# Performance work log

Measured on AMD Instinct MI355X. Metric: run time of the kernel, lower is better.

## Reference

```python
import jax, jax.numpy as jnp
import numpy as np

S, D = 16384, 1024


def setup_inputs() -> dict:
    key = jax.random.key(0)
    ks = jax.random.split(key, 7)
    stdv = 1.0 / np.sqrt(D)
    u = lambda k, shape: jax.random.uniform(k, shape, jnp.float32, -stdv, stdv)
    return {
        "x": jax.random.normal(ks[0], (S, D), jnp.float32),
        "Wq": u(ks[1], (D, D)), "bq": u(ks[2], (D,)),
        "Wk": u(ks[3], (D, D)), "bk": u(ks[4], (D,)),
        "Wv": u(ks[5], (D, D)), "bv": u(ks[6], (D,)),
    }


def reference(x, Wq, bq, Wk, bk, Wv, bv):
    # torch.nn.Linear: y = x @ W^T + b
    q = x @ Wq.T + bq          # [S, D]
    k = x @ Wk.T + bk          # [S, D]
    v = x @ Wv.T + bv          # [S, D]
    d = x.shape[-1]
    # NOTE: faithful to source -- scores are over the FEATURE axis: [D, D]
    scores = jnp.einsum('sd,se->de', q, k) / jnp.sqrt(jnp.float32(d))
    attn = jax.nn.softmax(scores, axis=-1)   # [D, D]
    out = v @ attn                           # [S, D]
    return out, attn
```

## Files before the change

### kernel.cpp

```cpp
#include <hip/hip_runtime.h>
#include <hip/hip_bf16.h>
#include <stdint.h>


#define S_ 16384
#define D_ 1024

typedef _Float16 half8 __attribute__((ext_vector_type(8)));
typedef _Float16 half4 __attribute__((ext_vector_type(4)));
typedef float f32x4 __attribute__((ext_vector_type(4)));

__device__ __forceinline__ void gload_lds16(const _Float16* g, _Float16* l) {
    __builtin_amdgcn_global_load_lds(
        (const __attribute__((address_space(1))) void*)g,
        (__attribute__((address_space(3))) void*)l, 16, 0, 0);
}

#define VM4() asm volatile("s_waitcnt vmcnt(4)" ::: "memory")
#define BARR() do { __builtin_amdgcn_s_barrier(); __builtin_amdgcn_sched_barrier(0); } while (0)
#define LGKM0() do { asm volatile("s_waitcnt lgkmcnt(0)" ::: "memory"); __builtin_amdgcn_sched_barrier(0); } while (0)

#define STAGEA(H, KT, NX) do { \
    const _Float16* _s = srcA + (size_t)((H) * 128) * lda + (size_t)(KT) * 64; \
    _Float16* _d = AsS + (NX) * 16384 + ((H) * 128 + 8 * w) * 64; \
    gload_lds16(_s, _d); \
    gload_lds16(_s + (size_t)64 * lda, _d + 4096); \
} while (0)

#define STAGEB(H, KT, NX) do { \
    const _Float16* _s = srcB + (size_t)((H) * 128) * ldb + (size_t)(KT) * 64; \
    _Float16* _d = BsS + (NX) * 16384 + ((H) * 128 + 8 * w) * 64; \
    gload_lds16(_s, _d); \
    gload_lds16(_s + (size_t)64 * ldb, _d + 4096); \
} while (0)

#define READA(QA) do { _Pragma("unroll") \
    for (int fm = 0; fm < 4; ++fm) { \
        af[fm][0] = *(const half8*)(pA + (((QA) * 64 + fm * 16) << 7) + cx0); \
        af[fm][1] = *(const half8*)(pA + (((QA) * 64 + fm * 16) << 7) + cx1); } \
} while (0)

#define READB(BF, QB) do { _Pragma("unroll") \
    for (int fn = 0; fn < 2; ++fn) { \
        BF[fn][0] = *(const half8*)(pB + (((QB) * 32 + fn * 16) << 7) + cx0); \
        BF[fn][1] = *(const half8*)(pB + (((QB) * 32 + fn * 16) << 7) + cx1); } \
} while (0)

#define MFMAB(QA, QB, BF) do { _Pragma("unroll") \
    for (int fm = 0; fm < 4; ++fm) { _Pragma("unroll") \
        for (int fn = 0; fn < 2; ++fn) { \
            f32x4 _c = acc[(QA) * 4 + fm][(QB) * 2 + fn]; \
            _c = __builtin_amdgcn_mfma_f32_16x16x32_f16(af[fm][0], BF[fn][0], _c, 0, 0, 0); \
            _c = __builtin_amdgcn_mfma_f32_16x16x32_f16(af[fm][1], BF[fn][1], _c, 0, 0, 0); \
            acc[(QA) * 4 + fm][(QB) * 2 + fn] = _c; } } \
} while (0)

template <int F16OUT, int BIAS>
__global__ __launch_bounds__(512, 2)
void gemm256(const _Float16* __restrict__ A, const _Float16* __restrict__ B,
             void* __restrict__ C, const float* __restrict__ bias,
             int lda, int ldb, int ldc, int ksub, long long mn,
             int ntx, int ntxy, int cpx) {
    __shared__ _Float16 As[2][16384];
    __shared__ _Float16 Bs[2][16384];
    const int t = threadIdx.x;
    const int l = t & 63;
    const int w = t >> 6;
    const int wm = w >> 2, wn = w & 3;

    const int hb = blockIdx.x;
    const int lg = (hb & 7) * cpx + (hb >> 3);
    const int bz = lg / ntxy;
    const int rem = lg - bz * ntxy;
    const int by = rem / ntx;
    const int bx = rem - by * ntx;
    const size_t m0 = (size_t)by * 256;
    const size_t n0 = (size_t)bx * 256;
    const size_t k0 = (size_t)bz * (size_t)ksub;
    const long long coff = (long long)bz * mn;

    const int colsw = 8 * ((l & 7) ^ (l >> 3));
    const _Float16* srcA = A + (m0 + 8 * w + (l >> 3)) * (size_t)lda + k0 + colsw;
    const _Float16* srcB = B + (n0 + 8 * w + (l >> 3)) * (size_t)ldb + k0 + colsw;
    _Float16* AsS = &As[0][0];
    _Float16* BsS = &Bs[0][0];

    const int cx0 = (((l >> 4) << 4)) ^ ((l & 7) << 4);
    const int cx1 = (64 + ((l >> 4) << 4)) ^ ((l & 7) << 4);
    const char* basePA = (const char*)AsS + (wm * 128 + (l & 15)) * 128;
    const char* basePB = (const char*)BsS + (wn * 64 + (l & 15)) * 128;

    f32x4 acc[8][4] = {};
    half8 af[4][2], bf0[2][2], bf1[2][2];

    const int nk = ksub >> 6;

    STAGEA(0, 0, 0); STAGEB(0, 0, 0); STAGEB(1, 0, 0); STAGEA(1, 0, 0);

    for (int kt = 0; kt < nk; ++kt) {
        const int p = kt & 1, nx = p ^ 1;
        const int ktn = kt + 1;
        const bool hn = ktn < nk;
        const char* pA = basePA + p * 32768;
        const char* pB = basePB + p * 32768;

        VM4(); BARR();
        READA(0); READB(bf0, 0);
        if (hn) STAGEA(0, ktn, nx);
        LGKM0();
        __builtin_amdgcn_s_setprio(1);
        MFMAB(0, 0, bf0);
        __builtin_amdgcn_s_setprio(0);

        VM4(); BARR();
        READB(bf1, 1);
        if (hn) STAGEB(0, ktn, nx);
        LGKM0();
        __builtin_amdgcn_s_setprio(1);
        MFMAB(0, 1, bf1);
        __builtin_amdgcn_s_setprio(0);

        VM4(); BARR();
        READA(1);
        if (hn) { STAGEB(1, ktn, nx); STAGEA(1, ktn, nx); }
        LGKM0();
        __builtin_amdgcn_s_setprio(1);
        MFMAB(1, 0, bf0);
        MFMAB(1, 1, bf1);
        __builtin_amdgcn_s_setprio(0);
    }

    const int cr = (l >> 4) << 2;
    const int cc = l & 15;
#pragma unroll
    for (int n = 0; n < 4; ++n) {
        const size_t col = n0 + wn * 64 + n * 16 + cc;
        const float bb = BIAS ? bias[col] : 0.f;
#pragma unroll
        for (int m = 0; m < 8; ++m) {
            const size_t row0 = m0 + wm * 128 + m * 16 + cr;
#pragma unroll
            for (int r = 0; r < 4; ++r) {
                const float val = acc[m][n][r] + bb;
                if (F16OUT)
                    ((_Float16*)C)[coff + (long long)(row0 + r) * ldc + col] = (_Float16)val;
                else
                    ((float*)C)[coff + (long long)(row0 + r) * ldc + col] = val;
            }
        }
    }
}

__global__ __launch_bounds__(256, 2)
void gemm_abt(const _Float16* __restrict__ A, const _Float16* __restrict__ B,
              float* __restrict__ C, const float* __restrict__ bias,
              int bias_mode, int lda, int ldb, int ldc, int ksub,
              float scale, long long mn) {
    const int t = threadIdx.x;
    const int lane = t & 63;
    const int wave = t >> 6;
    const int wr = (wave >> 1) * 64;
    const int wc = (wave & 1) * 64;
    const size_t m0 = (size_t)blockIdx.y * 128;
    const size_t n0 = (size_t)blockIdx.x * 128;
    const size_t k0 = (size_t)blockIdx.z * (size_t)ksub;
    const long long coff = (long long)blockIdx.z * mn;

    __shared__ _Float16 As[128 * 32];
    __shared__ _Float16 Bs[128 * 32];

    f32x4 acc[4][4] = {};

    const _Float16* a0 = A + (m0 + (size_t)(t >> 2)) * (size_t)lda + k0 + (t & 3) * 8;
    const _Float16* a1 = a0 + (size_t)64 * lda;
    const _Float16* b0 = B + (n0 + (size_t)(t >> 2)) * (size_t)ldb + k0 + (t & 3) * 8;
    const _Float16* b1 = b0 + (size_t)64 * ldb;
    _Float16* AsW0 = As + wave * 512;
    _Float16* AsW1 = As + 2048 + wave * 512;
    _Float16* BsW0 = Bs + wave * 512;
    _Float16* BsW1 = Bs + 2048 + wave * 512;

    const int nk = ksub >> 5;
    for (int kt = 0; kt < nk; ++kt) {
        __syncthreads();
        gload_lds16(a0, AsW0);
        gload_lds16(a1, AsW1);
        gload_lds16(b0, BsW0);
        gload_lds16(b1, BsW1);
        a0 += 32; a1 += 32; b0 += 32; b1 += 32;
        __syncthreads();

        half8 af[4], bf[4];
#pragma unroll
        for (int i = 0; i < 4; ++i)
            af[i] = *(const half8*)(As + (wr + i * 16 + (lane & 15)) * 32 + (lane >> 4) * 8);
#pragma unroll
        for (int i = 0; i < 4; ++i)
            bf[i] = *(const half8*)(Bs + (wc + i * 16 + (lane & 15)) * 32 + (lane >> 4) * 8);
#pragma unroll
        for (int i = 0; i < 4; ++i)
#pragma unroll
            for (int j = 0; j < 4; ++j)
                acc[i][j] = __builtin_amdgcn_mfma_f32_16x16x32_f16(af[i], bf[j], acc[i][j], 0, 0, 0);
    }

    const int cr = (lane >> 4) * 4;
    const int cc = lane & 15;
#pragma unroll
    for (int i = 0; i < 4; ++i) {
#pragma unroll
        for (int j = 0; j < 4; ++j) {
            const size_t row0 = m0 + wr + i * 16 + cr;
            const size_t col = n0 + wc + j * 16 + cc;
            const float bcol = (bias_mode == 2) ? bias[col] : 0.f;
#pragma unroll
            for (int r = 0; r < 4; ++r) {
                float val = acc[i][j][r] * scale + bcol;
                C[coff + (long long)(row0 + r) * ldc + col] = val;
            }
        }
    }
}

__global__ void cast_f32_f16(const float* __restrict__ in, _Float16* __restrict__ out, int n8) {
    int i = blockIdx.x * 256 + threadIdx.x;
    if (i >= n8) return;
    const f32x4* p = (const f32x4*)in + (size_t)i * 2;
    f32x4 x0 = p[0], x1 = p[1];
    half8 h;
    h[0] = (_Float16)x0[0]; h[1] = (_Float16)x0[1];
    h[2] = (_Float16)x0[2]; h[3] = (_Float16)x0[3];
    h[4] = (_Float16)x1[0]; h[5] = (_Float16)x1[1];
    h[6] = (_Float16)x1[2]; h[7] = (_Float16)x1[3];
    ((half8*)out)[i] = h;
}

template <int WRITE_ROW, int COLSUM>
__global__ __launch_bounds__(256)
void cast_transpose(const float* __restrict__ in, _Float16* __restrict__ outRow,
                    _Float16* __restrict__ outT, float* __restrict__ msum, int ldT) {
    __shared__ _Float16 tile[64][66];
    __shared__ float red[16][16][4];
    const int t = threadIdx.x;
    const int c0 = blockIdx.x * 64;
    const int r0 = blockIdx.y * 64;
    const int cg = t & 15;
    const int rb = t >> 4;
    f32x4 csum = {};
#pragma unroll
    for (int it = 0; it < 4; ++it) {
        const int rr = rb + it * 16;
        f32x4 v = *(const f32x4*)(in + (size_t)(r0 + rr) * 1024 + c0 + cg * 4);
        if (COLSUM) { csum[0] += v[0]; csum[1] += v[1]; csum[2] += v[2]; csum[3] += v[3]; }
        _Float16 h0 = (_Float16)v[0], h1 = (_Float16)v[1];
        _Float16 h2 = (_Float16)v[2], h3 = (_Float16)v[3];
        tile[rr][cg * 4 + 0] = h0; tile[rr][cg * 4 + 1] = h1;
        tile[rr][cg * 4 + 2] = h2; tile[rr][cg * 4 + 3] = h3;
        if (WRITE_ROW) {
            half4 h = {h0, h1, h2, h3};
            *(half4*)(outRow + (size_t)(r0 + rr) * 1024 + c0 + cg * 4) = h;
        }
    }
    if (COLSUM) {
        red[rb][cg][0] = csum[0]; red[rb][cg][1] = csum[1];
        red[rb][cg][2] = csum[2]; red[rb][cg][3] = csum[3];
    }
    __syncthreads();
    if (COLSUM && t < 64) {
        float s = 0.f;
#pragma unroll
        for (int k = 0; k < 16; ++k) s += red[k][t >> 2][t & 3];
        atomicAdd(msum + c0 + t, s);
    }
    const int i = t >> 2, ch = (t & 3) * 16;
    half8 h0v, h1v;
#pragma unroll
    for (int j = 0; j < 8; ++j) h0v[j] = tile[ch + j][i];
#pragma unroll
    for (int j = 0; j < 8; ++j) h1v[j] = tile[ch + 8 + j][i];
    *(half8*)(outT + (size_t)(c0 + i) * ldT + r0 + ch) = h0v;
    *(half8*)(outT + (size_t)(c0 + i) * ldT + r0 + ch + 8) = h1v;
}

__global__ void zero_vec(float* __restrict__ p, int n) {
    int i = blockIdx.x * 256 + threadIdx.x;
    if (i < n) p[i] = 0.f;
}

__global__ __launch_bounds__(256)
void u2w_kernel(const float* __restrict__ Wq, const float* __restrict__ Wk,
                const float* __restrict__ bq, const float* __restrict__ m,
                float* __restrict__ u2, float* __restrict__ w) {
    const int bid = blockIdx.x;
    const int t = threadIdx.x;
    const float* W = (bid < 1024) ? Wq : Wk;
    const int row = (bid < 1024) ? bid : bid - 1024;
    float s = 0.f;
#pragma unroll
    for (int it = 0; it < 4; ++it) {
        const int i = t + it * 256;
        s += W[(size_t)row * 1024 + i] * m[i];
    }
    for (int o = 32; o; o >>= 1) s += __shfl_xor(s, o);
    __shared__ float red[4];
    if ((t & 63) == 0) red[t >> 6] = s;
    __syncthreads();
    if (t == 0) {
        float tot = red[0] + red[1] + red[2] + red[3];
        if (bid < 1024) u2[bid] = tot + 16384.0f * bq[bid];
        else w[row] = tot;
    }
}

__global__ __launch_bounds__(256)
void reduce_g(const _Float16* __restrict__ part, _Float16* __restrict__ G16) {
    const size_t off = ((size_t)blockIdx.x * 256 + threadIdx.x) * 8;
    float s[8] = {};
    for (int z = 0; z < 16; ++z) {
        half8 v = *(const half8*)(part + (size_t)z * 1048576 + off);
#pragma unroll
        for (int j = 0; j < 8; ++j) s[j] += (float)v[j];
    }
    half8 o;
#pragma unroll
    for (int j = 0; j < 8; ++j) o[j] = (_Float16)s[j];
    *(half8*)(G16 + off) = o;
}

__global__ __launch_bounds__(256)
void reduce_cast(const float* __restrict__ part, _Float16* __restrict__ outh,
                 int nz, float scale) {
    const int idx = (blockIdx.x * 256 + threadIdx.x) * 4;
    f32x4 s = {};
    for (int z = 0; z < nz; ++z) {
        f32x4 v = *(const f32x4*)(part + (size_t)z * 1048576 + idx);
        s[0] += v[0]; s[1] += v[1]; s[2] += v[2]; s[3] += v[3];
    }
    half4 h;
    h[0] = (_Float16)(s[0] * scale); h[1] = (_Float16)(s[1] * scale);
    h[2] = (_Float16)(s[2] * scale); h[3] = (_Float16)(s[3] * scale);
    *(half4*)(outh + idx) = h;
}

__global__ __launch_bounds__(256)
void softmax_rows(const float* __restrict__ part, const float* __restrict__ u2,
                  const float* __restrict__ bq, const float* __restrict__ bk,
                  const float* __restrict__ w,
                  float* __restrict__ P, _Float16* __restrict__ PT) {
    const int a = blockIdx.x;
    const int t = threadIdx.x;
    __shared__ float red[8];
    const size_t off = (size_t)a * 1024 + t * 4;
    f32x4 s = {};
#pragma unroll
    for (int z = 0; z < 4; ++z) {
        f32x4 v = *(const f32x4*)(part + (size_t)z * 1048576 + off);
        s[0] += v[0]; s[1] += v[1]; s[2] += v[2]; s[3] += v[3];
    }
    const float ru = u2[a], rb = bq[a];
    f32x4 bk4 = *(const f32x4*)(bk + t * 4);
    f32x4 w4 = *(const f32x4*)(w + t * 4);
#pragma unroll
    for (int j = 0; j < 4; ++j) s[j] = (s[j] + ru * bk4[j] + rb * w4[j]) * 0.03125f;

    float m = fmaxf(fmaxf(s[0], s[1]), fmaxf(s[2], s[3]));
    for (int o = 32; o; o >>= 1) m = fmaxf(m, __shfl_xor(m, o));
    if ((t & 63) == 0) red[t >> 6] = m;
    __syncthreads();
    m = fmaxf(fmaxf(red[0], red[1]), fmaxf(red[2], red[3]));

    float e0 = expf(s[0] - m), e1 = expf(s[1] - m);
    float e2 = expf(s[2] - m), e3 = expf(s[3] - m);
    float sum = e0 + e1 + e2 + e3;
    for (int o = 32; o; o >>= 1) sum += __shfl_xor(sum, o);
    if ((t & 63) == 0) red[4 + (t >> 6)] = sum;
    __syncthreads();
    sum = red[4] + red[5] + red[6] + red[7];
    const float inv = 1.0f / sum;

    f32x4 o4 = {e0 * inv, e1 * inv, e2 * inv, e3 * inv};
    *(f32x4*)(P + off) = o4;
    const int b = t * 4;
    PT[(size_t)(b + 0) * 1024 + a] = (_Float16)o4[0];
    PT[(size_t)(b + 1) * 1024 + a] = (_Float16)o4[1];
    PT[(size_t)(b + 2) * 1024 + a] = (_Float16)o4[2];
    PT[(size_t)(b + 3) * 1024 + a] = (_Float16)o4[3];
}

__global__ __launch_bounds__(256)
void attn_bv(const float* __restrict__ attn, const float* __restrict__ bv,
             float* __restrict__ c) {
    const int j = blockIdx.x * 256 + threadIdx.x;
    const int a0 = blockIdx.y * 64;
    float s = 0.f;
#pragma unroll 4
    for (int k = 0; k < 64; ++k) {
        const int a = a0 + k;
        s += attn[(size_t)a * 1024 + j] * bv[a];
    }
    atomicAdd(c + j, s);
}

extern "C" void kernel_launch(void* const* d_in, const int* in_sizes, int n_in,
                              void* d_out, int out_size, void* d_ws, size_t ws_size,
                              hipStream_t stream) {
    const float* x  = (const float*)d_in[0];
    const float* Wq = (const float*)d_in[1];
    const float* bq = (const float*)d_in[2];
    const float* Wk = (const float*)d_in[3];
    const float* bk = (const float*)d_in[4];
    const float* Wv = (const float*)d_in[5];
    const float* bv = (const float*)d_in[6];
    float* out  = (float*)d_out;
    float* attn = out + (size_t)S_ * D_;

    char* ws = (char*)d_ws;
    float*    part  = (float*)ws;
    _Float16* partH = (_Float16*)ws;
    _Float16* x16   = (_Float16*)(ws + 33554432);
    _Float16* xT16  = (_Float16*)(ws + 67108864);
    _Float16* wq16  = (_Float16*)(ws + 100663296);
    _Float16* wk16  = (_Float16*)(ws + 102760448);
    _Float16* wvT16 = (_Float16*)(ws + 104857600);
    _Float16* G16   = (_Float16*)(ws + 106954752);
    _Float16* U16   = (_Float16*)(ws + 109051904);
    _Float16* PT    = (_Float16*)(ws + 111149056);
    _Float16* MT16  = (_Float16*)(ws + 113246208);
    float*    mvec  = (float*)(ws + 115343360);
    float*    u2    = mvec + 1024;
    float*    wv    = u2 + 1024;
    float*    cvec  = wv + 1024;

    zero_vec<<<16, 256, 0, stream>>>(mvec, 4096);
    cast_transpose<1, 1><<<dim3(16, 256), 256, 0, stream>>>(x, x16, xT16, mvec, S_);
    cast_f32_f16<<<512, 256, 0, stream>>>(Wq, wq16, D_ * D_ / 8);
    cast_f32_f16<<<512, 256, 0, stream>>>(Wk, wk16, D_ * D_ / 8);
    cast_transpose<0, 0><<<dim3(16, 16), 256, 0, stream>>>(Wv, nullptr, wvT16, nullptr, D_);
    u2w_kernel<<<2048, 256, 0, stream>>>(Wq, Wk, bq, mvec, u2, wv);

    gemm256<1, 0><<<256, 512, 0, stream>>>(xT16, xT16, (void*)partH, nullptr,
                                           16384, 16384, 1024, 1024, 1048576LL,
                                           4, 16, 32);
    reduce_g<<<512, 256, 0, stream>>>(partH, G16);
    gemm_abt<<<dim3(8, 8, 4), 256, 0, stream>>>(wq16, G16, part, nullptr, 0,
                                                1024, 1024, 1024, 256, 1.0f, 1048576);
    reduce_cast<<<1024, 256, 0, stream>>>(part, U16, 4, 1.0f);
    gemm_abt<<<dim3(8, 8, 4), 256, 0, stream>>>(U16, wk16, part, nullptr, 0,
                                                1024, 1024, 1024, 256, 1.0f, 1048576);
    softmax_rows<<<1024, 256, 0, stream>>>(part, u2, bq, bk, wv, attn, PT);
    attn_bv<<<dim3(4, 16), 256, 0, stream>>>(attn, bv, cvec);
    gemm_abt<<<dim3(8, 8, 4), 256, 0, stream>>>(PT, wvT16, part, nullptr, 0,
                                                1024, 1024, 1024, 256, 1.0f, 1048576);
    reduce_cast<<<1024, 256, 0, stream>>>(part, MT16, 4, 1.0f);
    gemm256<0, 1><<<256, 512, 0, stream>>>(x16, MT16, (void*)out, cvec,
                                           1024, 1024, 1024, 1024, 0LL,
                                           4, 256, 32);
}
```

Measured before the change: 192.3 us.

## Deepen gemm256 prefetch to two k-tiles, interleave warp tiles, merge weight casts

The 256x256 GEMM now stages two k-tiles ahead instead of one and reuses the just-consumed buffer for the stage after next. The schedule changes to extra barriers, a vmcnt(8) wait and a reordered MFMA sequence that reuses bf1 before reloading A. The per-wave fragment layout changes from contiguous 128x64 blocks to interleaved 64x32 sub-tiles, so LDS read addresses and the epilogue index math change with it. The two Wq/Wk cast launches are merged into one kernel. Together these aim to hide global-load latency better and cut one launch, at the cost of more barriers and a correctness risk from overwriting a buffer that may still be read.

```diff
diff --git a/kernel.cpp b/kernel.cpp
--- a/kernel.cpp
+++ b/kernel.cpp
@@ -16,9 +16,12 @@
         (__attribute__((address_space(3))) void*)l, 16, 0, 0);
 }
 
-#define VM4() asm volatile("s_waitcnt vmcnt(4)" ::: "memory")
-#define BARR() do { __builtin_amdgcn_s_barrier(); __builtin_amdgcn_sched_barrier(0); } while (0)
+#define VM8() do { asm volatile("s_waitcnt vmcnt(8)" ::: "memory"); __builtin_amdgcn_sched_barrier(0); } while (0)
+#define VM0() do { asm volatile("s_waitcnt vmcnt(0)" ::: "memory"); __builtin_amdgcn_sched_barrier(0); } while (0)
+#define BAR() __builtin_amdgcn_s_barrier()
 #define LGKM0() do { asm volatile("s_waitcnt lgkmcnt(0)" ::: "memory"); __builtin_amdgcn_sched_barrier(0); } while (0)
+#define PRIO1() __builtin_amdgcn_s_setprio(1)
+#define PRIO0() __builtin_amdgcn_s_setprio(0)
 
 #define STAGEA(H, KT, NX) do { \
     const _Float16* _s = srcA + (size_t)((H) * 128) * lda + (size_t)(KT) * 64; \
@@ -34,16 +37,16 @@
     gload_lds16(_s + (size_t)64 * ldb, _d + 4096); \
 } while (0)
 
-#define READA(QA) do { _Pragma("unroll") \
+#define READA(PA, QA) do { _Pragma("unroll") \
     for (int fm = 0; fm < 4; ++fm) { \
-        af[fm][0] = *(const half8*)(pA + (((QA) * 64 + fm * 16) << 7) + cx0); \
-        af[fm][1] = *(const half8*)(pA + (((QA) * 64 + fm * 16) << 7) + cx1); } \
+        af[fm][0] = *(const half8*)((PA) + (((QA) * 128 + fm * 16) << 7) + cx0); \
+        af[fm][1] = *(const half8*)((PA) + (((QA) * 128 + fm * 16) << 7) + cx1); } \
 } while (0)
 
-#define READB(BF, QB) do { _Pragma("unroll") \
+#define READB(PB, BF, QB) do { _Pragma("unroll") \
     for (int fn = 0; fn < 2; ++fn) { \
-        BF[fn][0] = *(const half8*)(pB + (((QB) * 32 + fn * 16) << 7) + cx0); \
-        BF[fn][1] = *(const half8*)(pB + (((QB) * 32 + fn * 16) << 7) + cx1); } \
+        BF[fn][0] = *(const half8*)((PB) + (((QB) * 128 + fn * 16) << 7) + cx0); \
+        BF[fn][1] = *(const half8*)((PB) + (((QB) * 128 + fn * 16) << 7) + cx1); } \
 } while (0)
 
 #define MFMAB(QA, QB, BF) do { _Pragma("unroll") \
@@ -87,8 +90,8 @@
 
     const int cx0 = (((l >> 4) << 4)) ^ ((l & 7) << 4);
     const int cx1 = (64 + ((l >> 4) << 4)) ^ ((l & 7) << 4);
-    const char* basePA = (const char*)AsS + (wm * 128 + (l & 15)) * 128;
-    const char* basePB = (const char*)BsS + (wn * 64 + (l & 15)) * 128;
+    const char* basePA = (const char*)AsS + ((wm * 64 + (l & 15)) << 7);
+    const char* basePB = (const char*)BsS + ((wn * 32 + (l & 15)) << 7);
 
     f32x4 acc[8][4] = {};
     half8 af[4][2], bf0[2][2], bf1[2][2];
@@ -96,49 +99,45 @@
     const int nk = ksub >> 6;
 
     STAGEA(0, 0, 0); STAGEB(0, 0, 0); STAGEB(1, 0, 0); STAGEA(1, 0, 0);
+    STAGEA(0, 1, 1); STAGEB(0, 1, 1); STAGEB(1, 1, 1); STAGEA(1, 1, 1);
 
     for (int kt = 0; kt < nk; ++kt) {
-        const int p = kt & 1, nx = p ^ 1;
-        const int ktn = kt + 1;
-        const bool hn = ktn < nk;
+        const int p = kt & 1;
+        const int ks = kt + 2;
+        const bool hs = ks < nk;
         const char* pA = basePA + p * 32768;
         const char* pB = basePB + p * 32768;
 
-        VM4(); BARR();
-        READA(0); READB(bf0, 0);
-        if (hn) STAGEA(0, ktn, nx);
-        LGKM0();
-        __builtin_amdgcn_s_setprio(1);
-        MFMAB(0, 0, bf0);
-        __builtin_amdgcn_s_setprio(0);
-
-        VM4(); BARR();
-        READB(bf1, 1);
-        if (hn) STAGEB(0, ktn, nx);
-        LGKM0();
-        __builtin_amdgcn_s_setprio(1);
-        MFMAB(0, 1, bf1);
-        __builtin_amdgcn_s_setprio(0);
-
-        VM4(); BARR();
-        READA(1);
-        if (hn) { STAGEB(1, ktn, nx); STAGEA(1, ktn, nx); }
-        LGKM0();
-        __builtin_amdgcn_s_setprio(1);
-        MFMAB(1, 0, bf0);
-        MFMAB(1, 1, bf1);
-        __builtin_amdgcn_s_setprio(0);
+        if (kt == nk - 1) VM0(); else VM8();
+        BAR();
+
+        READA(pA, 0); READB(pB, bf0, 0);
+        BAR(); LGKM0();
+        PRIO1(); MFMAB(0, 0, bf0); PRIO0(); BAR();
+
+        READB(pB, bf1, 1);
+        if (hs) { STAGEA(0, ks, p); STAGEB(0, ks, p); }
+        BAR(); LGKM0();
+        PRIO1(); MFMAB(0, 1, bf1); PRIO0(); BAR();
+
+        READA(pA, 1);
+        if (hs) STAGEB(1, ks, p);
+        BAR(); LGKM0();
+        PRIO1(); MFMAB(1, 1, bf1); PRIO0(); BAR();
+
+        if (hs) STAGEA(1, ks, p);
+        PRIO1(); MFMAB(1, 0, bf0); PRIO0(); BAR();
     }
 
     const int cr = (l >> 4) << 2;
     const int cc = l & 15;
 #pragma unroll
     for (int n = 0; n < 4; ++n) {
-        const size_t col = n0 + wn * 64 + n * 16 + cc;
+        const size_t col = n0 + (n >> 1) * 128 + wn * 32 + (n & 1) * 16 + cc;
         const float bb = BIAS ? bias[col] : 0.f;
 #pragma unroll
         for (int m = 0; m < 8; ++m) {
-            const size_t row0 = m0 + wm * 128 + m * 16 + cr;
+            const size_t row0 = m0 + (m >> 2) * 128 + wm * 64 + (m & 3) * 16 + cr;
 #pragma unroll
             for (int r = 0; r < 4; ++r) {
                 const float val = acc[m][n][r] + bb;
@@ -222,9 +221,13 @@
     }
 }
 
-__global__ void cast_f32_f16(const float* __restrict__ in, _Float16* __restrict__ out, int n8) {
+__global__ void cast2_f32_f16(const float* __restrict__ inA, _Float16* __restrict__ outA,
+                              const float* __restrict__ inB, _Float16* __restrict__ outB,
+                              int n8) {
     int i = blockIdx.x * 256 + threadIdx.x;
-    if (i >= n8) return;
+    const float* in = inA;
+    _Float16* out = outA;
+    if (i >= n8) { i -= n8; in = inB; out = outB; }
     const f32x4* p = (const f32x4*)in + (size_t)i * 2;
     f32x4 x0 = p[0], x1 = p[1];
     half8 h;
@@ -433,8 +436,7 @@
 
     zero_vec<<<16, 256, 0, stream>>>(mvec, 4096);
     cast_transpose<1, 1><<<dim3(16, 256), 256, 0, stream>>>(x, x16, xT16, mvec, S_);
-    cast_f32_f16<<<512, 256, 0, stream>>>(Wq, wq16, D_ * D_ / 8);
-    cast_f32_f16<<<512, 256, 0, stream>>>(Wk, wk16, D_ * D_ / 8);
+    cast2_f32_f16<<<1024, 256, 0, stream>>>(Wq, wq16, Wk, wk16, D_ * D_ / 8);
     cast_transpose<0, 0><<<dim3(16, 16), 256, 0, stream>>>(Wv, nullptr, wvT16, nullptr, D_);
     u2w_kernel<<<2048, 256, 0, stream>>>(Wq, Wk, bq, mvec, u2, wv);
 
```

Result: slower. 198.2 us (+3.1%).
